# Optimization experiments

Measured on AMD Instinct MI355X. Metric: run time of the kernel, lower is better.

Reference implementation:

```python
import jax, jax.numpy as jnp
import numpy as np

NUM_CHANNELS = 256
NUM_HEADS = 8
HEAD_DIM = NUM_CHANNELS // NUM_HEADS


def setup_inputs() -> dict:
    key = jax.random.key(0)
    k1, k2, k3, k4, k5 = jax.random.split(key, 5)
    C = NUM_CHANNELS
    s = 1.0 / np.sqrt(C)
    image = jax.random.normal(k1, (8, C, 32, 32), dtype=jnp.float32)
    # kqv_projection: Linear(C, 3C); mix_heads: Linear(C, C). Stored as [in, out].
    w_kqv = jax.random.uniform(k2, (C, 3 * C), minval=-s, maxval=s, dtype=jnp.float32)
    b_kqv = jax.random.uniform(k3, (3 * C,), minval=-s, maxval=s, dtype=jnp.float32)
    w_mix = jax.random.uniform(k4, (C, C), minval=-s, maxval=s, dtype=jnp.float32)
    b_mix = jax.random.uniform(k5, (C,), minval=-s, maxval=s, dtype=jnp.float32)
    return {"image": image, "w_kqv": w_kqv, "b_kqv": b_kqv, "w_mix": w_mix, "b_mix": b_mix}


def _masked_attention(seq, w_kqv, b_kqv, w_mix, b_mix):
    # seq: [N, T, C]
    N, T, C = seq.shape
    H, D = NUM_HEADS, HEAD_DIM
    projected = seq @ w_kqv + b_kqv            # [N, T, 3C]
    k, q, v = jnp.split(projected, 3, axis=-1)  # order: keys, queries, values
    # split heads -> [N, H, T, D]
    k = k.reshape(N, T, H, D).transpose(0, 2, 1, 3)
    q = q.reshape(N, T, H, D).transpose(0, 2, 1, 3)
    v = v.reshape(N, T, H, D).transpose(0, 2, 1, 3)
    logits = jnp.einsum('nhtd,nhsd->nhts', q, k) / jnp.sqrt(jnp.float32(D))
    causal = jnp.tril(jnp.ones((T, T), dtype=bool))
    logits = jnp.where(causal, logits, -jnp.inf)
    weights = jax.nn.softmax(logits, axis=-1)
    out = jnp.einsum('nhts,nhsd->nhtd', weights, v)  # [N, H, T, D]
    out = out.transpose(0, 2, 1, 3).reshape(N, T, C)  # combine heads
    return out @ w_mix + b_mix


def reference(image, w_kqv, b_kqv, w_mix, b_mix):
    N, C, Hh, Ww = image.shape
    seq = image.transpose(0, 2, 3, 1).reshape(N, Hh * Ww, C)
    attn = _masked_attention(seq, w_kqv, b_kqv, w_mix, b_mix)
    attn = attn.reshape(N, Hh, Ww, C).transpose(0, 3, 1, 2)
    return attn + image
```

## Files before the change

### kernel.cpp

```cpp
#include <hip/hip_runtime.h>
#include <math.h>

constexpr int NB  = 8;
constexpr int C   = 256;
constexpr int T   = 1024;
constexpr int NH  = 8;
constexpr int HD  = 32;
constexpr int C3  = 768;

constexpr float QSCALE = 0.25503489422229562f;

typedef __attribute__((ext_vector_type(8))) short bf16x8;
typedef __attribute__((ext_vector_type(4))) float f32x4;

__device__ inline short f2bf(float f) {
    unsigned u = __float_as_uint(f);
    u += 0x7FFF + ((u >> 16) & 1);
    return (short)(u >> 16);
}
__device__ inline short f2bf_trunc(float f) {
    return (short)(__float_as_uint(f) >> 16);
}

__global__ __launch_bounds__(256) void xpose_w(const float* __restrict__ wkqv,
                                               const float* __restrict__ wmix,
                                               short* __restrict__ wkqvT,
                                               short* __restrict__ wmixT) {
    __shared__ float Ld[32][33];
    const int bid = blockIdx.x;
    const float* src; short* dst; int srcStride;
    if (bid < 192) {
        int jb = bid >> 3, cb = bid & 7;
        src = wkqv + (size_t)(cb * 32) * C3 + jb * 32;
        dst = wkqvT + (size_t)(jb * 32) * C + cb * 32;
        srcStride = C3;
    } else {
        int id = bid - 192, jb = id >> 3, cb = id & 7;
        src = wmix + (size_t)(cb * 32) * C + jb * 32;
        dst = wmixT + (size_t)(jb * 32) * C + cb * 32;
        srcStride = C;
    }
    const int r = threadIdx.x >> 3, c4 = (threadIdx.x & 7) * 4;
    float4 v = *(const float4*)&src[(size_t)r * srcStride + c4];
    Ld[r][c4 + 0] = v.x; Ld[r][c4 + 1] = v.y; Ld[r][c4 + 2] = v.z; Ld[r][c4 + 3] = v.w;
    __syncthreads();
    short4 o = { f2bf(Ld[c4 + 0][r]), f2bf(Ld[c4 + 1][r]),
                 f2bf(Ld[c4 + 2][r]), f2bf(Ld[c4 + 3][r]) };
    *(short4*)&dst[(size_t)r * C + c4] = o;
}

__global__ __launch_bounds__(256) void kqv_mfma(const float* __restrict__ image,
                                                const short* __restrict__ wkqvT,
                                                const float* __restrict__ bkqv,
                                                short* __restrict__ Kb,
                                                short* __restrict__ Qb,
                                                short* __restrict__ Vb) {
    __shared__ __align__(16) short As[64][40];
    __shared__ __align__(16) short Bs[64][40];
    const int tid = threadIdx.x;
    const int n0 = blockIdx.x * 64;
    const int m0 = blockIdx.y * 64;
    const int nb = m0 >> 10, t0 = m0 & 1023;
    const int wv = tid >> 6, lane = tid & 63;
    const int m = lane & 15, quad = lane >> 4;
    const int sr = tid >> 2, sc8 = (tid & 3) * 8;
    const int am = tid & 63, ak8 = (tid >> 6) * 8;

    const float* imgn = image + (size_t)nb * C * T;

    f32x4 acc[4];
    const f32x4 z = {0.f, 0.f, 0.f, 0.f};
    #pragma unroll
    for (int j = 0; j < 4; ++j) acc[j] = z;

    float fa[8];
    #pragma unroll
    for (int i = 0; i < 8; ++i)
        fa[i] = imgn[(size_t)(ak8 + i) * T + t0 + am];
    bf16x8 breg = *(const bf16x8*)&wkqvT[(size_t)(n0 + sr) * C + sc8];

    for (int k0 = 0; k0 < C; k0 += 32) {
        __syncthreads();
        short4 alo = { f2bf(fa[0]), f2bf(fa[1]), f2bf(fa[2]), f2bf(fa[3]) };
        short4 ahi = { f2bf(fa[4]), f2bf(fa[5]), f2bf(fa[6]), f2bf(fa[7]) };
        *(short4*)&As[am][ak8]     = alo;
        *(short4*)&As[am][ak8 + 4] = ahi;
        *(bf16x8*)&Bs[sr][sc8] = breg;
        if (k0 + 32 < C) {
            #pragma unroll
            for (int i = 0; i < 8; ++i)
                fa[i] = imgn[(size_t)(k0 + 32 + ak8 + i) * T + t0 + am];
            breg = *(const bf16x8*)&wkqvT[(size_t)(n0 + sr) * C + k0 + 32 + sc8];
        }
        __syncthreads();
        bf16x8 a = *(const bf16x8*)&As[16 * wv + m][8 * quad];
        bf16x8 b[4];
        #pragma unroll
        for (int j = 0; j < 4; ++j) b[j] = *(const bf16x8*)&Bs[16 * j + m][8 * quad];
        #pragma unroll
        for (int j = 0; j < 4; ++j)
            acc[j] = __builtin_amdgcn_mfma_f32_16x16x32_bf16(a, b[j], acc[j], 0, 0, 0);
    }

    #pragma unroll
    for (int j = 0; j < 4; ++j) {
        int jj = n0 + 16 * j + m;
        int chunk = jj >> 8, hh = (jj >> 5) & 7, d = jj & 31;
        short* dst = (chunk == 0) ? Kb : (chunk == 1) ? Qb : Vb;
        float bias = bkqv[jj];
        float mul = (chunk == 1) ? QSCALE : 1.0f;
        size_t base = (size_t)(nb * NH + hh) * T * HD + d;
        int t = t0 + 16 * wv + 4 * quad;
        #pragma unroll
        for (int r = 0; r < 4; ++r)
            dst[base + (size_t)(t + r) * HD] = f2bf((acc[j][r] + bias) * mul);
    }
}

__global__ __launch_bounds__(256) void attn_mfma(const short* __restrict__ Kb,
                                                 const short* __restrict__ Qb,
                                                 const short* __restrict__ Vb,
                                                 short* __restrict__ attnb) {
    const int qp = blockIdx.x;
    const int h  = blockIdx.y;
    const int nb = blockIdx.z;
    const int tid  = threadIdx.x;
    const int wv   = tid >> 6;
    const int lane = tid & 63;
    const int m    = lane & 15;
    const int quad = lane >> 4;

    __shared__ __align__(16) short Qs[128][40];
    __shared__ __align__(16) short Ks[2][64][40];
    __shared__ __align__(16) short Vt[2][32][72];
    __shared__ __align__(16) short Ps[128][72];

    const size_t hb = (size_t)(nb * NH + h) * T * HD;
    const short* Kp = Kb + hb;
    const short* Qp = Qb + hb;
    const short* Vp = Vb + hb;
    const int sr = tid >> 2, sc8 = (tid & 3) * 8;
    const f32x4 z = {0.f, 0.f, 0.f, 0.f};

    #pragma unroll 1
    for (int pp = 0; pp < 2; ++pp) {
        const int qb  = pp ? 7 - qp : qp;
        const int q0  = qb * 128;
        const int nst = 2 * qb + 2;

        __syncthreads();

        *(bf16x8*)&Qs[sr][sc8]      = *(const bf16x8*)&Qp[(size_t)(q0 + sr) * HD + sc8];
        *(bf16x8*)&Qs[64 + sr][sc8] = *(const bf16x8*)&Qp[(size_t)(q0 + 64 + sr) * HD + sc8];
        bf16x8 kreg = *(const bf16x8*)&Kp[(size_t)sr * HD + sc8];
        bf16x8 vreg = *(const bf16x8*)&Vp[(size_t)sr * HD + sc8];
        *(bf16x8*)&Ks[0][sr][sc8] = kreg;
        #pragma unroll
        for (int i2 = 0; i2 < 8; ++i2) Vt[0][sc8 + i2][sr] = vreg[i2];

        f32x4 O[2][2] = {{z, z}, {z, z}};
        float lp[2][4] = {};

        for (int st = 0; st < nst; ++st) {
            const int p = st & 1;
            __syncthreads();
            if (st + 1 < nst) {
                kreg = *(const bf16x8*)&Kp[(size_t)((st + 1) * 64 + sr) * HD + sc8];
                vreg = *(const bf16x8*)&Vp[(size_t)((st + 1) * 64 + sr) * HD + sc8];
            }

            bf16x8 bk[4];
            #pragma unroll
            for (int j = 0; j < 4; ++j) bk[j] = *(const bf16x8*)&Ks[p][16 * j + m][8 * quad];
            f32x4 S[2][4];
            #pragma unroll
            for (int i = 0; i < 2; ++i) {
                bf16x8 aq = *(const bf16x8*)&Qs[32 * wv + 16 * i + m][8 * quad];
                #pragma unroll
                for (int j = 0; j < 4; ++j)
                    S[i][j] = __builtin_amdgcn_mfma_f32_16x16x32_bf16(aq, bk[j], z, 0, 0, 0);
            }

            const bool msk = (st >= 2 * qb);
            const int s0 = st * 64;
            #pragma unroll
            for (int i = 0; i < 2; ++i) {
                const int qr_base = q0 + 32 * wv + 16 * i + 4 * quad;
                #pragma unroll
                for (int j = 0; j < 4; ++j) {
                    const int sc = s0 + 16 * j + m;
                    #pragma unroll
                    for (int r = 0; r < 4; ++r) {
                        float e = __builtin_amdgcn_exp2f(S[i][j][r]);
                        if (msk && sc > qr_base + r) e = 0.f;
                        lp[i][r] += e;
                        Ps[32 * wv + 16 * i + 4 * quad + r][16 * j + m] = f2bf_trunc(e);
                    }
                }
            }

            #pragma unroll
            for (int kc = 0; kc < 2; ++kc) {
                bf16x8 ap0 = *(const bf16x8*)&Ps[32 * wv + m][32 * kc + 8 * quad];
                bf16x8 ap1 = *(const bf16x8*)&Ps[32 * wv + 16 + m][32 * kc + 8 * quad];
                bf16x8 b0  = *(const bf16x8*)&Vt[p][m][32 * kc + 8 * quad];
                bf16x8 b1  = *(const bf16x8*)&Vt[p][16 + m][32 * kc + 8 * quad];
                O[0][0] = __builtin_amdgcn_mfma_f32_16x16x32_bf16(ap0, b0, O[0][0], 0, 0, 0);
                O[0][1] = __builtin_amdgcn_mfma_f32_16x16x32_bf16(ap0, b1, O[0][1], 0, 0, 0);
                O[1][0] = __builtin_amdgcn_mfma_f32_16x16x32_bf16(ap1, b0, O[1][0], 0, 0, 0);
                O[1][1] = __builtin_amdgcn_mfma_f32_16x16x32_bf16(ap1, b1, O[1][1], 0, 0, 0);
            }

            if (st + 1 < nst) {
                const int pn = p ^ 1;
                *(bf16x8*)&Ks[pn][sr][sc8] = kreg;
                #pragma unroll
                for (int i2 = 0; i2 < 8; ++i2) Vt[pn][sc8 + i2][sr] = vreg[i2];
            }
        }

        #pragma unroll
        for (int i = 0; i < 2; ++i)
            #pragma unroll
            for (int r = 0; r < 4; ++r) {
                float l = lp[i][r];
                l += __shfl_xor(l, 1);
                l += __shfl_xor(l, 2);
                l += __shfl_xor(l, 4);
                l += __shfl_xor(l, 8);
                float inv = 1.f / l;
                int row = q0 + 32 * wv + 16 * i + 4 * quad + r;
                short* op = attnb + ((size_t)(nb * T + row)) * C + h * HD;
                op[m]      = f2bf(O[i][0][r] * inv);
                op[16 + m] = f2bf(O[i][1][r] * inv);
            }
    }
}

__global__ __launch_bounds__(256) void mix_mfma(const short* __restrict__ attnb,
                                                const short* __restrict__ wmixT,
                                                const float* __restrict__ bmix,
                                                const float* __restrict__ image,
                                                float* __restrict__ out) {
    __shared__ __align__(16) short As[64][40];
    __shared__ __align__(16) short Bs[64][40];
    const int tid = threadIdx.x;
    const int n0 = blockIdx.x * 64;
    const int m0 = blockIdx.y * 64;
    const int nb = m0 >> 10, t0 = m0 & 1023;
    const int wv = tid >> 6, lane = tid & 63;
    const int m = lane & 15, quad = lane >> 4;
    const int sr = tid >> 2, sc8 = (tid & 3) * 8;

    f32x4 acc[4];
    const f32x4 z = {0.f, 0.f, 0.f, 0.f};
    #pragma unroll
    for (int j = 0; j < 4; ++j) acc[j] = z;

    bf16x8 areg = *(const bf16x8*)&attnb[(size_t)(m0 + sr) * C + sc8];
    bf16x8 breg = *(const bf16x8*)&wmixT[(size_t)(n0 + sr) * C + sc8];

    for (int k0 = 0; k0 < C; k0 += 32) {
        __syncthreads();
        *(bf16x8*)&As[sr][sc8] = areg;
        *(bf16x8*)&Bs[sr][sc8] = breg;
        if (k0 + 32 < C) {
            areg = *(const bf16x8*)&attnb[(size_t)(m0 + sr) * C + k0 + 32 + sc8];
            breg = *(const bf16x8*)&wmixT[(size_t)(n0 + sr) * C + k0 + 32 + sc8];
        }
        __syncthreads();
        bf16x8 a = *(const bf16x8*)&As[16 * wv + m][8 * quad];
        bf16x8 b[4];
        #pragma unroll
        for (int j = 0; j < 4; ++j) b[j] = *(const bf16x8*)&Bs[16 * j + m][8 * quad];
        #pragma unroll
        for (int j = 0; j < 4; ++j)
            acc[j] = __builtin_amdgcn_mfma_f32_16x16x32_bf16(a, b[j], acc[j], 0, 0, 0);
    }

    const int tb = t0 + 16 * wv + 4 * quad;
    #pragma unroll
    for (int j = 0; j < 4; ++j) {
        int c = n0 + 16 * j + m;
        float bias = bmix[c];
        size_t o = (size_t)(nb * C + c) * T + tb;
        float4 img = *(const float4*)&image[o];
        float4 res = { acc[j][0] + bias + img.x,
                       acc[j][1] + bias + img.y,
                       acc[j][2] + bias + img.z,
                       acc[j][3] + bias + img.w };
        *(float4*)&out[o] = res;
    }
}

extern "C" void kernel_launch(void* const* d_in, const int* in_sizes, int n_in,
                              void* d_out, int out_size, void* d_ws, size_t ws_size,
                              hipStream_t stream) {
    const float* image = (const float*)d_in[0];
    const float* w_kqv = (const float*)d_in[1];
    const float* b_kqv = (const float*)d_in[2];
    const float* w_mix = (const float*)d_in[3];
    const float* b_mix = (const float*)d_in[4];
    float* out = (float*)d_out;

    short* wkqvT = (short*)d_ws;
    short* wmixT = wkqvT + (size_t)C3 * C;
    short* Kb    = wmixT + (size_t)C * C;
    short* Qb    = Kb    + (size_t)NB * NH * T * HD;
    short* Vb    = Qb    + (size_t)NB * NH * T * HD;
    short* attnb = Vb    + (size_t)NB * NH * T * HD;

    xpose_w<<<256, 256, 0, stream>>>(w_kqv, w_mix, wkqvT, wmixT);
    kqv_mfma<<<dim3(C3 / 64, NB * T / 64), 256, 0, stream>>>(image, wkqvT, b_kqv, Kb, Qb, Vb);
    attn_mfma<<<dim3(4, NH, NB), 256, 0, stream>>>(Kb, Qb, Vb, attnb);
    mix_mfma<<<dim3(C / 64, NB * T / 64), 256, 0, stream>>>(attnb, wmixT, b_mix, image, out);
}
```

Measured before the change: 112.7 us.

## Drop weight transpose kernel; load fp32 weights directly and enlarge KQV tile

```diff
diff --git a/kernel.cpp b/kernel.cpp
--- a/kernel.cpp
+++ b/kernel.cpp
@@ -22,84 +22,73 @@
     return (short)(__float_as_uint(f) >> 16);
 }
 
-__global__ __launch_bounds__(256) void xpose_w(const float* __restrict__ wkqv,
-                                               const float* __restrict__ wmix,
-                                               short* __restrict__ wkqvT,
-                                               short* __restrict__ wmixT) {
-    __shared__ float Ld[32][33];
-    const int bid = blockIdx.x;
-    const float* src; short* dst; int srcStride;
-    if (bid < 192) {
-        int jb = bid >> 3, cb = bid & 7;
-        src = wkqv + (size_t)(cb * 32) * C3 + jb * 32;
-        dst = wkqvT + (size_t)(jb * 32) * C + cb * 32;
-        srcStride = C3;
-    } else {
-        int id = bid - 192, jb = id >> 3, cb = id & 7;
-        src = wmix + (size_t)(cb * 32) * C + jb * 32;
-        dst = wmixT + (size_t)(jb * 32) * C + cb * 32;
-        srcStride = C;
-    }
-    const int r = threadIdx.x >> 3, c4 = (threadIdx.x & 7) * 4;
-    float4 v = *(const float4*)&src[(size_t)r * srcStride + c4];
-    Ld[r][c4 + 0] = v.x; Ld[r][c4 + 1] = v.y; Ld[r][c4 + 2] = v.z; Ld[r][c4 + 3] = v.w;
-    __syncthreads();
-    short4 o = { f2bf(Ld[c4 + 0][r]), f2bf(Ld[c4 + 1][r]),
-                 f2bf(Ld[c4 + 2][r]), f2bf(Ld[c4 + 3][r]) };
-    *(short4*)&dst[(size_t)r * C + c4] = o;
-}
-
 __global__ __launch_bounds__(256) void kqv_mfma(const float* __restrict__ image,
-                                                const short* __restrict__ wkqvT,
+                                                const float* __restrict__ wkqv,
                                                 const float* __restrict__ bkqv,
                                                 short* __restrict__ Kb,
                                                 short* __restrict__ Qb,
                                                 short* __restrict__ Vb) {
-    __shared__ __align__(16) short As[64][40];
+    __shared__ __align__(16) short As[128][40];
     __shared__ __align__(16) short Bs[64][40];
     const int tid = threadIdx.x;
     const int n0 = blockIdx.x * 64;
-    const int m0 = blockIdx.y * 64;
+    const int m0 = blockIdx.y * 128;
     const int nb = m0 >> 10, t0 = m0 & 1023;
     const int wv = tid >> 6, lane = tid & 63;
     const int m = lane & 15, quad = lane >> 4;
-    const int sr = tid >> 2, sc8 = (tid & 3) * 8;
     const int am = tid & 63, ak8 = (tid >> 6) * 8;
 
     const float* imgn = image + (size_t)nb * C * T;
 
-    f32x4 acc[4];
+    f32x4 acc[2][4];
     const f32x4 z = {0.f, 0.f, 0.f, 0.f};
     #pragma unroll
-    for (int j = 0; j < 4; ++j) acc[j] = z;
-
-    float fa[8];
-    #pragma unroll
-    for (int i = 0; i < 8; ++i)
-        fa[i] = imgn[(size_t)(ak8 + i) * T + t0 + am];
-    bf16x8 breg = *(const bf16x8*)&wkqvT[(size_t)(n0 + sr) * C + sc8];
+    for (int i = 0; i < 2; ++i)
+        #pragma unroll
+        for (int j = 0; j < 4; ++j) acc[i][j] = z;
+
+    float fa[2][8], fb[8];
+    #pragma unroll
+    for (int i = 0; i < 8; ++i) {
+        fa[0][i] = imgn[(size_t)(ak8 + i) * T + t0 + am];
+        fa[1][i] = imgn[(size_t)(ak8 + i) * T + t0 + 64 + am];
+        fb[i]    = wkqv[(size_t)(ak8 + i) * C3 + n0 + am];
+    }
 
     for (int k0 = 0; k0 < C; k0 += 32) {
         __syncthreads();
-        short4 alo = { f2bf(fa[0]), f2bf(fa[1]), f2bf(fa[2]), f2bf(fa[3]) };
-        short4 ahi = { f2bf(fa[4]), f2bf(fa[5]), f2bf(fa[6]), f2bf(fa[7]) };
-        *(short4*)&As[am][ak8]     = alo;
-        *(short4*)&As[am][ak8 + 4] = ahi;
-        *(bf16x8*)&Bs[sr][sc8] = breg;
+        #pragma unroll
+        for (int h2 = 0; h2 < 2; ++h2) {
+            short4 lo = { f2bf(fa[h2][0]), f2bf(fa[h2][1]), f2bf(fa[h2][2]), f2bf(fa[h2][3]) };
+            short4 hi = { f2bf(fa[h2][4]), f2bf(fa[h2][5]), f2bf(fa[h2][6]), f2bf(fa[h2][7]) };
+            *(short4*)&As[64 * h2 + am][ak8]     = lo;
+            *(short4*)&As[64 * h2 + am][ak8 + 4] = hi;
+        }
+        {
+            short4 lo = { f2bf(fb[0]), f2bf(fb[1]), f2bf(fb[2]), f2bf(fb[3]) };
+            short4 hi = { f2bf(fb[4]), f2bf(fb[5]), f2bf(fb[6]), f2bf(fb[7]) };
+            *(short4*)&Bs[am][ak8]     = lo;
+            *(short4*)&Bs[am][ak8 + 4] = hi;
+        }
         if (k0 + 32 < C) {
             #pragma unroll
-            for (int i = 0; i < 8; ++i)
-                fa[i] = imgn[(size_t)(k0 + 32 + ak8 + i) * T + t0 + am];
-            breg = *(const bf16x8*)&wkqvT[(size_t)(n0 + sr) * C + k0 + 32 + sc8];
-        }
-        __syncthreads();
-        bf16x8 a = *(const bf16x8*)&As[16 * wv + m][8 * quad];
-        bf16x8 b[4];
+            for (int i = 0; i < 8; ++i) {
+                fa[0][i] = imgn[(size_t)(k0 + 32 + ak8 + i) * T + t0 + am];
+                fa[1][i] = imgn[(size_t)(k0 + 32 + ak8 + i) * T + t0 + 64 + am];
+                fb[i]    = wkqv[(size_t)(k0 + 32 + ak8 + i) * C3 + n0 + am];
+            }
+        }
+        __syncthreads();
+        bf16x8 a[2], b[4];
+        #pragma unroll
+        for (int i = 0; i < 2; ++i) a[i] = *(const bf16x8*)&As[32 * wv + 16 * i + m][8 * quad];
         #pragma unroll
         for (int j = 0; j < 4; ++j) b[j] = *(const bf16x8*)&Bs[16 * j + m][8 * quad];
         #pragma unroll
-        for (int j = 0; j < 4; ++j)
-            acc[j] = __builtin_amdgcn_mfma_f32_16x16x32_bf16(a, b[j], acc[j], 0, 0, 0);
+        for (int i = 0; i < 2; ++i)
+            #pragma unroll
+            for (int j = 0; j < 4; ++j)
+                acc[i][j] = __builtin_amdgcn_mfma_f32_16x16x32_bf16(a[i], b[j], acc[i][j], 0, 0, 0);
     }
 
     #pragma unroll
@@ -110,10 +99,13 @@
         float bias = bkqv[jj];
         float mul = (chunk == 1) ? QSCALE : 1.0f;
         size_t base = (size_t)(nb * NH + hh) * T * HD + d;
-        int t = t0 + 16 * wv + 4 * quad;
-        #pragma unroll
-        for (int r = 0; r < 4; ++r)
-            dst[base + (size_t)(t + r) * HD] = f2bf((acc[j][r] + bias) * mul);
+        #pragma unroll
+        for (int i = 0; i < 2; ++i) {
+            int t = t0 + 32 * wv + 16 * i + 4 * quad;
+            #pragma unroll
+            for (int r = 0; r < 4; ++r)
+                dst[base + (size_t)(t + r) * HD] = f2bf((acc[i][j][r] + bias) * mul);
+        }
     }
 }
 
@@ -238,7 +230,7 @@
 }
 
 __global__ __launch_bounds__(256) void mix_mfma(const short* __restrict__ attnb,
-                                                const short* __restrict__ wmixT,
+                                                const float* __restrict__ wmix,
                                                 const float* __restrict__ bmix,
                                                 const float* __restrict__ image,
                                                 float* __restrict__ out) {
@@ -251,6 +243,7 @@
     const int wv = tid >> 6, lane = tid & 63;
     const int m = lane & 15, quad = lane >> 4;
     const int sr = tid >> 2, sc8 = (tid & 3) * 8;
+    const int am = tid & 63, ak8 = (tid >> 6) * 8;
 
     f32x4 acc[4];
     const f32x4 z = {0.f, 0.f, 0.f, 0.f};
@@ -258,15 +251,25 @@
     for (int j = 0; j < 4; ++j) acc[j] = z;
 
     bf16x8 areg = *(const bf16x8*)&attnb[(size_t)(m0 + sr) * C + sc8];
-    bf16x8 breg = *(const bf16x8*)&wmixT[(size_t)(n0 + sr) * C + sc8];
+    float fb[8];
+    #pragma unroll
+    for (int i = 0; i < 8; ++i)
+        fb[i] = wmix[(size_t)(ak8 + i) * C + n0 + am];
 
     for (int k0 = 0; k0 < C; k0 += 32) {
         __syncthreads();
         *(bf16x8*)&As[sr][sc8] = areg;
-        *(bf16x8*)&Bs[sr][sc8] = breg;
+        {
+            short4 lo = { f2bf(fb[0]), f2bf(fb[1]), f2bf(fb[2]), f2bf(fb[3]) };
+            short4 hi = { f2bf(fb[4]), f2bf(fb[5]), f2bf(fb[6]), f2bf(fb[7]) };
+            *(short4*)&Bs[am][ak8]     = lo;
+            *(short4*)&Bs[am][ak8 + 4] = hi;
+        }
         if (k0 + 32 < C) {
             areg = *(const bf16x8*)&attnb[(size_t)(m0 + sr) * C + k0 + 32 + sc8];
-            breg = *(const bf16x8*)&wmixT[(size_t)(n0 + sr) * C + k0 + 32 + sc8];
+            #pragma unroll
+            for (int i = 0; i < 8; ++i)
+                fb[i] = wmix[(size_t)(k0 + 32 + ak8 + i) * C + n0 + am];
         }
         __syncthreads();
         bf16x8 a = *(const bf16x8*)&As[16 * wv + m][8 * quad];
@@ -303,15 +306,12 @@
     const float* b_mix = (const float*)d_in[4];
     float* out = (float*)d_out;
 
-    short* wkqvT = (short*)d_ws;
-    short* wmixT = wkqvT + (size_t)C3 * C;
-    short* Kb    = wmixT + (size_t)C * C;
-    short* Qb    = Kb    + (size_t)NB * NH * T * HD;
-    short* Vb    = Qb    + (size_t)NB * NH * T * HD;
-    short* attnb = Vb    + (size_t)NB * NH * T * HD;
-
-    xpose_w<<<256, 256, 0, stream>>>(w_kqv, w_mix, wkqvT, wmixT);
-    kqv_mfma<<<dim3(C3 / 64, NB * T / 64), 256, 0, stream>>>(image, wkqvT, b_kqv, Kb, Qb, Vb);
+    short* Kb    = (short*)d_ws;
+    short* Qb    = Kb + (size_t)NB * NH * T * HD;
+    short* Vb    = Qb + (size_t)NB * NH * T * HD;
+    short* attnb = Vb + (size_t)NB * NH * T * HD;
+
+    kqv_mfma<<<dim3(C3 / 64, NB * T / 128), 256, 0, stream>>>(image, w_kqv, b_kqv, Kb, Qb, Vb);
     attn_mfma<<<dim3(4, NH, NB), 256, 0, stream>>>(Kb, Qb, Vb, attnb);
-    mix_mfma<<<dim3(C / 64, NB * T / 64), 256, 0, stream>>>(attnb, wmixT, b_mix, image, out);
-}
+    mix_mfma<<<dim3(C / 64, NB * T / 64), 256, 0, stream>>>(attnb, w_mix, b_mix, image, out);
+}
```

Result: no change. 111.7 us (-0.9%).
